# Kernel optimization log

Measured on AMD Instinct MI355X. Metric: run time of the kernel, lower is better.

Reference implementation:

```python
import jax, jax.numpy as jnp
import numpy as np

N_HEAD = 16
N_EMBD = 2048
B, S = 2, 2048


def setup_inputs() -> dict:
    key = jax.random.key(0)
    k1, k2, k3 = jax.random.split(key, 3)
    scale = 0.02
    return {
        "hidden_states": jax.random.normal(k1, (B, S, N_EMBD), dtype=jnp.float32),
        "attention_mask": jnp.ones((B, S), dtype=jnp.float32),
        "w_attn": jax.random.normal(k2, (N_EMBD, 3 * N_EMBD), dtype=jnp.float32) * scale,
        "b_attn": jnp.zeros((3 * N_EMBD,), dtype=jnp.float32),
        "w_proj": jax.random.normal(k3, (N_EMBD, N_EMBD), dtype=jnp.float32) * scale,
        "b_proj": jnp.zeros((N_EMBD,), dtype=jnp.float32),
    }


def reference(hidden_states, attention_mask, w_attn, b_attn, w_proj, b_proj):
    b, s, d = hidden_states.shape
    h = N_HEAD
    dh = d // h
    qkv = hidden_states @ w_attn + b_attn          # [b, s, 3d]
    q, k, v = jnp.split(qkv, 3, axis=-1)
    # [b, s, d] -> [b, h, s, dh]
    q = q.reshape(b, s, h, dh).transpose(0, 2, 1, 3)
    k = k.reshape(b, s, h, dh).transpose(0, 2, 1, 3)
    v = v.reshape(b, s, h, dh).transpose(0, 2, 1, 3)
    scores = jnp.einsum("bhqd,bhkd->bhqk", q, k) / jnp.sqrt(jnp.float32(dh))
    # padding mask: [b, s] -> additive bias [b, 1, 1, s]
    bias = (1.0 - attention_mask)[:, None, None, :] * -10000.0
    attn = jax.nn.softmax(scores + bias, axis=-1)   # dropout p=0 (eval)
    out = jnp.einsum("bhqk,bhkd->bhqd", attn, v)    # [b, h, s, dh]
    out = out.transpose(0, 2, 1, 3).reshape(b, s, d)
    return out @ w_proj + b_proj
```

## Files before the change

### kernel.cpp

```cpp
#include <hip/hip_runtime.h>
#include <stdint.h>

#define B_   2
#define S_   2048
#define D_   2048
#define NH_  16
#define DH_  128
#define N3_  6144

typedef unsigned short u16;
typedef __bf16 bf16x8 __attribute__((ext_vector_type(8)));
typedef float  f32x4  __attribute__((ext_vector_type(4)));

__device__ __forceinline__ u16 f2bf(float f) {
  union { float f; unsigned u; } v; v.f = f;
  unsigned u = v.u;
  return (u16)((u + 0x7FFFu + ((u >> 16) & 1u)) >> 16);
}

#define GL2LDS(gsrc, ldst)                                                              \
  __builtin_amdgcn_global_load_lds((const __attribute__((address_space(1))) void*)(gsrc), \
      (__attribute__((address_space(3))) void*)(ldst), 16, 0, 0)

__global__ void cvt_kernel(const float* __restrict__ in, u16* __restrict__ out, int n4) {
  int i = blockIdx.x * blockDim.x + threadIdx.x;
  int stride = gridDim.x * blockDim.x;
  for (; i < n4; i += stride) {
    float4 v = ((const float4*)in)[i];
    ushort4 o;
    o.x = f2bf(v.x); o.y = f2bf(v.y); o.z = f2bf(v.z); o.w = f2bf(v.w);
    ((ushort4*)out)[i] = o;
  }
}

__global__ void transpose_kernel(const float* __restrict__ in, u16* __restrict__ out,
                                 int K, int N) {
  __shared__ float tile[32][33];
  int tx = threadIdx.x, ty = threadIdx.y;
  int nx = blockIdx.x * 32, ky = blockIdx.y * 32;
#pragma unroll
  for (int j = 0; j < 32; j += 8)
    tile[ty + j][tx] = in[(size_t)(ky + ty + j) * N + nx + tx];
  __syncthreads();
#pragma unroll
  for (int j = 0; j < 32; j += 8)
    out[(size_t)(nx + ty + j) * K + ky + tx] = f2bf(tile[tx][ty + j]);
}

template <int KD>
__device__ __forceinline__ void gemm_core(const u16* __restrict__ A,
                                          const u16* __restrict__ BT,
                                          int m0, int n0, u16* As, u16* Bs,
                                          f32x4 acc[4][4]) {
  int t = threadIdx.x;
  int lane = t & 63, wv = t >> 6;
  int g = lane >> 4, lr = lane & 15;
  int wr = wv >> 1, wc = wv & 1;
  for (int k0 = 0; k0 < KD; k0 += 64) {
#pragma unroll
    for (int i = 0; i < 4; ++i) {
      int idx = i * 256 + t;
      int row = idx >> 3, slot = idx & 7;
      GL2LDS(A + (size_t)(m0 + row) * KD + k0 + ((slot ^ (row & 7)) * 8), As + idx * 8);
    }
#pragma unroll
    for (int i = 0; i < 4; ++i) {
      int idx = i * 256 + t;
      int row = idx >> 3, slot = idx & 7;
      GL2LDS(BT + (size_t)(n0 + row) * KD + k0 + ((slot ^ (row & 7)) * 8), Bs + idx * 8);
    }
    __syncthreads();
#pragma unroll
    for (int kk = 0; kk < 2; ++kk) {
      bf16x8 af[4], bfr[4];
#pragma unroll
      for (int m = 0; m < 4; ++m) {
        int r = wr * 64 + m * 16 + lr;
        af[m] = *reinterpret_cast<const bf16x8*>(As + r * 64 + ((((kk << 2) | g) ^ (r & 7)) * 8));
      }
#pragma unroll
      for (int n = 0; n < 4; ++n) {
        int r = wc * 64 + n * 16 + lr;
        bfr[n] = *reinterpret_cast<const bf16x8*>(Bs + r * 64 + ((((kk << 2) | g) ^ (r & 7)) * 8));
      }
#pragma unroll
      for (int m = 0; m < 4; ++m)
#pragma unroll
        for (int n = 0; n < 4; ++n)
          acc[m][n] = __builtin_amdgcn_mfma_f32_16x16x32_bf16(af[m], bfr[n], acc[m][n], 0, 0, 0);
    }
    __syncthreads();
  }
}

__global__ __launch_bounds__(256) void gemm_qkv_kernel(
    const u16* __restrict__ A, const u16* __restrict__ BT, const float* __restrict__ bias,
    u16* __restrict__ Qb, u16* __restrict__ Kb, u16* __restrict__ VTb) {
  __shared__ __attribute__((aligned(16))) u16 As[128 * 64];
  __shared__ __attribute__((aligned(16))) u16 Bs[128 * 64];
  f32x4 acc[4][4] = {};
  int m0 = blockIdx.y * 128, n0 = blockIdx.x * 128;
  gemm_core<2048>(A, BT, m0, n0, As, Bs, acc);
  int t = threadIdx.x, lane = t & 63, wv = t >> 6;
  int g = lane >> 4, lr = lane & 15, wr = wv >> 1, wc = wv & 1;
#pragma unroll
  for (int m = 0; m < 4; ++m) {
    int rowbase = m0 + wr * 64 + m * 16 + g * 4;
    int b = rowbase >> 11, s = rowbase & 2047;
#pragma unroll
    for (int n = 0; n < 4; ++n) {
      int col = n0 + wc * 64 + n * 16 + lr;
      float bv = bias[col];
      int sec = col >> 11;
      int within = col & 2047;
      int h = within >> 7, d = within & 127;
      if (sec < 2) {
        u16* dst = (sec == 0 ? Qb : Kb) + ((size_t)(b * NH_ + h) * S_ + s) * DH_ + d;
#pragma unroll
        for (int r = 0; r < 4; ++r) dst[(size_t)r * DH_] = f2bf(acc[m][n][r] + bv);
      } else {
        u16* dst = VTb + ((size_t)(b * NH_ + h) * DH_ + d) * S_ + s;
        ushort4 pk;
        pk.x = f2bf(acc[m][n][0] + bv); pk.y = f2bf(acc[m][n][1] + bv);
        pk.z = f2bf(acc[m][n][2] + bv); pk.w = f2bf(acc[m][n][3] + bv);
        *reinterpret_cast<ushort4*>(dst) = pk;
      }
    }
  }
}

__global__ __launch_bounds__(256) void gemm_proj_kernel(
    const u16* __restrict__ A, const u16* __restrict__ BT, const float* __restrict__ bias,
    float* __restrict__ out) {
  __shared__ __attribute__((aligned(16))) u16 As[128 * 64];
  __shared__ __attribute__((aligned(16))) u16 Bs[128 * 64];
  f32x4 acc[4][4] = {};
  int m0 = blockIdx.y * 128, n0 = blockIdx.x * 128;
  gemm_core<2048>(A, BT, m0, n0, As, Bs, acc);
  int t = threadIdx.x, lane = t & 63, wv = t >> 6;
  int g = lane >> 4, lr = lane & 15, wr = wv >> 1, wc = wv & 1;
#pragma unroll
  for (int m = 0; m < 4; ++m) {
    int rowbase = m0 + wr * 64 + m * 16 + g * 4;
#pragma unroll
    for (int n = 0; n < 4; ++n) {
      int col = n0 + wc * 64 + n * 16 + lr;
      float bv = bias[col];
      float* dst = out + (size_t)rowbase * D_ + col;
#pragma unroll
      for (int r = 0; r < 4; ++r) dst[(size_t)r * D_] = acc[m][n][r] + bv;
    }
  }
}

__global__ __launch_bounds__(256) void attn_kernel(
    const u16* __restrict__ Qb, const u16* __restrict__ Kb, const u16* __restrict__ VTb,
    const float* __restrict__ mask, u16* __restrict__ AO) {
  __shared__ __attribute__((aligned(16))) u16 Ks[64 * 128];
  __shared__ __attribute__((aligned(16))) u16 Vs[128 * 64];
  __shared__ __attribute__((aligned(16))) u16 Ps[4][16 * 64];
  int t = threadIdx.x, w = t >> 6, lane = t & 63;
  int g = lane >> 4, lr = lane & 15;
  int qt = blockIdx.x, bh = blockIdx.y;
  int b = bh >> 4, h = bh & 15;
  const u16* Qh = Qb + (size_t)bh * S_ * DH_;
  const u16* Kh = Kb + (size_t)bh * S_ * DH_;
  const u16* Vh = VTb + (size_t)bh * DH_ * S_;
  int q0 = qt * 64 + w * 16;

  bf16x8 aq[4];
#pragma unroll
  for (int kk = 0; kk < 4; ++kk)
    aq[kk] = *reinterpret_cast<const bf16x8*>(Qh + (size_t)(q0 + lr) * DH_ + kk * 32 + g * 8);

  f32x4 oacc[8] = {};
  float m_r[4], l_r[4];
#pragma unroll
  for (int r = 0; r < 4; ++r) { m_r[r] = -1e30f; l_r[r] = 0.f; }
  const float sc = 0.08838834764831845f;

  for (int s0 = 0; s0 < S_; s0 += 64) {
#pragma unroll
    for (int i = 0; i < 4; ++i) {
      int idx = i * 256 + t;
      int row = idx >> 4, slot = idx & 15;
      GL2LDS(Kh + (size_t)(s0 + row) * DH_ + ((slot ^ (row & 7)) * 8), Ks + idx * 8);
    }
#pragma unroll
    for (int i = 0; i < 4; ++i) {
      int idx = i * 256 + t;
      int row = idx >> 3, slot = idx & 7;
      GL2LDS(Vh + (size_t)row * S_ + s0 + ((slot ^ (row & 7)) * 8), Vs + idx * 8);
    }
    __syncthreads();

    f32x4 sacc[4] = {};
#pragma unroll
    for (int kk = 0; kk < 4; ++kk) {
#pragma unroll
      for (int n = 0; n < 4; ++n) {
        int c = lr + 16 * n;
        bf16x8 bk = *reinterpret_cast<const bf16x8*>(
            Ks + c * 128 + ((((kk << 2) | g) ^ (c & 7)) * 8));
        sacc[n] = __builtin_amdgcn_mfma_f32_16x16x32_bf16(aq[kk], bk, sacc[n], 0, 0, 0);
      }
    }

    float bias_n[4];
#pragma unroll
    for (int n = 0; n < 4; ++n)
      bias_n[n] = (1.0f - mask[b * S_ + s0 + lr + 16 * n]) * -10000.0f;

#pragma unroll
    for (int r = 0; r < 4; ++r) {
      float sv[4];
#pragma unroll
      for (int n = 0; n < 4; ++n) sv[n] = sacc[n][r] * sc + bias_n[n];
      float mx = fmaxf(fmaxf(sv[0], sv[1]), fmaxf(sv[2], sv[3]));
#pragma unroll
      for (int off = 1; off < 16; off <<= 1) mx = fmaxf(mx, __shfl_xor(mx, off));
      float mnew = fmaxf(m_r[r], mx);
      float f = __expf(m_r[r] - mnew);
      m_r[r] = mnew;
      float sum = 0.f;
      u16 pb[4];
#pragma unroll
      for (int n = 0; n < 4; ++n) { float p = __expf(sv[n] - mnew); sum += p; pb[n] = f2bf(p); }
#pragma unroll
      for (int off = 1; off < 16; off <<= 1) sum += __shfl_xor(sum, off);
      l_r[r] = l_r[r] * f + sum;
#pragma unroll
      for (int no = 0; no < 8; ++no) oacc[no][r] *= f;
      int prow = g * 4 + r;
#pragma unroll
      for (int n = 0; n < 4; ++n) {
        int col = lr + 16 * n;
        Ps[w][prow * 64 + ((((col >> 3) ^ (prow & 7)) << 3) + (col & 7))] = pb[n];
      }
    }

#pragma unroll
    for (int kk2 = 0; kk2 < 2; ++kk2) {
      bf16x8 ap = *reinterpret_cast<const bf16x8*>(
          &Ps[w][lr * 64 + ((((kk2 << 2) | g) ^ (lr & 7)) * 8)]);
#pragma unroll
      for (int no = 0; no < 8; ++no) {
        int d = lr + 16 * no;
        bf16x8 bv = *reinterpret_cast<const bf16x8*>(
            Vs + d * 64 + ((((kk2 << 2) | g) ^ (d & 7)) * 8));
        oacc[no] = __builtin_amdgcn_mfma_f32_16x16x32_bf16(ap, bv, oacc[no], 0, 0, 0);
      }
    }
    __syncthreads();
  }

#pragma unroll
  for (int r = 0; r < 4; ++r) {
    float inv = 1.0f / l_r[r];
    int qrow = q0 + g * 4 + r;
    u16* dst = AO + ((size_t)(b * S_ + qrow)) * D_ + h * DH_;
#pragma unroll
    for (int no = 0; no < 8; ++no) dst[lr + 16 * no] = f2bf(oacc[no][r] * inv);
  }
}

extern "C" void kernel_launch(void* const* d_in, const int* in_sizes, int n_in,
                              void* d_out, int out_size, void* d_ws, size_t ws_size,
                              hipStream_t stream) {
  const float* h_in   = (const float*)d_in[0];
  const float* mask   = (const float*)d_in[1];
  const float* w_attn = (const float*)d_in[2];
  const float* b_attn = (const float*)d_in[3];
  const float* w_proj = (const float*)d_in[4];
  const float* b_proj = (const float*)d_in[5];
  float* out = (float*)d_out;

  char* ws = (char*)d_ws;
  u16* Hb  = (u16*)(ws);
  u16* W1T = (u16*)(ws + 16777216);
  u16* W2T = (u16*)(ws + 41943040);
  u16* Qb  = (u16*)(ws + 50331648);
  u16* Kb  = (u16*)(ws + 67108864);
  u16* VTb = (u16*)(ws + 83886080);
  u16* AO  = Hb;

  cvt_kernel<<<2048, 256, 0, stream>>>(h_in, Hb, (B_ * S_ * D_) / 4);
  dim3 tb(32, 8);
  transpose_kernel<<<dim3(N3_ / 32, D_ / 32), tb, 0, stream>>>(w_attn, W1T, D_, N3_);
  transpose_kernel<<<dim3(D_ / 32, D_ / 32), tb, 0, stream>>>(w_proj, W2T, D_, D_);
  gemm_qkv_kernel<<<dim3(N3_ / 128, (B_ * S_) / 128), 256, 0, stream>>>(
      Hb, W1T, b_attn, Qb, Kb, VTb);
  attn_kernel<<<dim3(S_ / 64, B_ * NH_), 256, 0, stream>>>(Qb, Kb, VTb, mask, AO);
  gemm_proj_kernel<<<dim3(D_ / 128, (B_ * S_) / 128), 256, 0, stream>>>(AO, W2T, b_proj, out);
}
```

Before: 482.3 us.

## Double-buffer K/V in attention, fold scale into Q, lazy softmax rescale, swizzle blocks

```diff
diff --git a/kernel.cpp b/kernel.cpp
--- a/kernel.cpp
+++ b/kernel.cpp
@@ -12,15 +12,30 @@
 typedef __bf16 bf16x8 __attribute__((ext_vector_type(8)));
 typedef float  f32x4  __attribute__((ext_vector_type(4)));
 
+#define QSCALE   (0.08838834764831845f * 1.4426950408889634f)
+#define BIASF    (-10000.0f * 1.4426950408889634f)
+
 __device__ __forceinline__ u16 f2bf(float f) {
   union { float f; unsigned u; } v; v.f = f;
   unsigned u = v.u;
   return (u16)((u + 0x7FFFu + ((u >> 16) & 1u)) >> 16);
 }
 
+__device__ __forceinline__ float fast_exp2(float x) {
+  float r;
+  asm("v_exp_f32 %0, %1" : "=v"(r) : "v"(x));
+  return r;
+}
+
 #define GL2LDS(gsrc, ldst)                                                              \
   __builtin_amdgcn_global_load_lds((const __attribute__((address_space(1))) void*)(gsrc), \
       (__attribute__((address_space(3))) void*)(ldst), 16, 0, 0)
+
+__device__ __forceinline__ int swz_id() {
+  int id = blockIdx.y * gridDim.x + blockIdx.x;
+  int cpx = (gridDim.x * gridDim.y) >> 3;
+  return (id & 7) * cpx + (id >> 3);
+}
 
 __global__ void cvt_kernel(const float* __restrict__ in, u16* __restrict__ out, int n4) {
   int i = blockIdx.x * blockDim.x + threadIdx.x;
@@ -99,7 +114,8 @@
   __shared__ __attribute__((aligned(16))) u16 As[128 * 64];
   __shared__ __attribute__((aligned(16))) u16 Bs[128 * 64];
   f32x4 acc[4][4] = {};
-  int m0 = blockIdx.y * 128, n0 = blockIdx.x * 128;
+  int sw = swz_id();
+  int n0 = (sw % gridDim.x) * 128, m0 = (sw / gridDim.x) * 128;
   gemm_core<2048>(A, BT, m0, n0, As, Bs, acc);
   int t = threadIdx.x, lane = t & 63, wv = t >> 6;
   int g = lane >> 4, lr = lane & 15, wr = wv >> 1, wc = wv & 1;
@@ -115,9 +131,10 @@
       int within = col & 2047;
       int h = within >> 7, d = within & 127;
       if (sec < 2) {
+        float mult = (sec == 0) ? QSCALE : 1.0f;
         u16* dst = (sec == 0 ? Qb : Kb) + ((size_t)(b * NH_ + h) * S_ + s) * DH_ + d;
 #pragma unroll
-        for (int r = 0; r < 4; ++r) dst[(size_t)r * DH_] = f2bf(acc[m][n][r] + bv);
+        for (int r = 0; r < 4; ++r) dst[(size_t)r * DH_] = f2bf((acc[m][n][r] + bv) * mult);
       } else {
         u16* dst = VTb + ((size_t)(b * NH_ + h) * DH_ + d) * S_ + s;
         ushort4 pk;
@@ -135,7 +152,8 @@
   __shared__ __attribute__((aligned(16))) u16 As[128 * 64];
   __shared__ __attribute__((aligned(16))) u16 Bs[128 * 64];
   f32x4 acc[4][4] = {};
-  int m0 = blockIdx.y * 128, n0 = blockIdx.x * 128;
+  int sw = swz_id();
+  int n0 = (sw % gridDim.x) * 128, m0 = (sw / gridDim.x) * 128;
   gemm_core<2048>(A, BT, m0, n0, As, Bs, acc);
   int t = threadIdx.x, lane = t & 63, wv = t >> 6;
   int g = lane >> 4, lr = lane & 15, wr = wv >> 1, wc = wv & 1;
@@ -156,18 +174,24 @@
 __global__ __launch_bounds__(256) void attn_kernel(
     const u16* __restrict__ Qb, const u16* __restrict__ Kb, const u16* __restrict__ VTb,
     const float* __restrict__ mask, u16* __restrict__ AO) {
-  __shared__ __attribute__((aligned(16))) u16 Ks[64 * 128];
-  __shared__ __attribute__((aligned(16))) u16 Vs[128 * 64];
+  __shared__ __attribute__((aligned(16))) u16 Ks[2][64 * 128];
+  __shared__ __attribute__((aligned(16))) u16 Vs[2][128 * 64];
   __shared__ __attribute__((aligned(16))) u16 Ps[4][16 * 64];
+  __shared__ float bias_lds[S_];
+
   int t = threadIdx.x, w = t >> 6, lane = t & 63;
   int g = lane >> 4, lr = lane & 15;
-  int qt = blockIdx.x, bh = blockIdx.y;
-  int b = bh >> 4, h = bh & 15;
+  int sw = swz_id();
+  int qt = sw & 31, bh = sw >> 5;
+  int b = bh >> 4;
   const u16* Qh = Qb + (size_t)bh * S_ * DH_;
   const u16* Kh = Kb + (size_t)bh * S_ * DH_;
   const u16* Vh = VTb + (size_t)bh * DH_ * S_;
   int q0 = qt * 64 + w * 16;
 
+  for (int i = t; i < S_; i += 256)
+    bias_lds[i] = (1.0f - mask[b * S_ + i]) * BIASF;
+
   bf16x8 aq[4];
 #pragma unroll
   for (int kk = 0; kk < 4; ++kk)
@@ -177,22 +201,39 @@
   float m_r[4], l_r[4];
 #pragma unroll
   for (int r = 0; r < 4; ++r) { m_r[r] = -1e30f; l_r[r] = 0.f; }
-  const float sc = 0.08838834764831845f;
-
-  for (int s0 = 0; s0 < S_; s0 += 64) {
-#pragma unroll
-    for (int i = 0; i < 4; ++i) {
-      int idx = i * 256 + t;
-      int row = idx >> 4, slot = idx & 15;
-      GL2LDS(Kh + (size_t)(s0 + row) * DH_ + ((slot ^ (row & 7)) * 8), Ks + idx * 8);
-    }
-#pragma unroll
-    for (int i = 0; i < 4; ++i) {
-      int idx = i * 256 + t;
-      int row = idx >> 3, slot = idx & 7;
-      GL2LDS(Vh + (size_t)row * S_ + s0 + ((slot ^ (row & 7)) * 8), Vs + idx * 8);
-    }
-    __syncthreads();
+
+  __syncthreads();
+
+#define STAGE_KV(buf, s0base)                                                    \
+  {                                                                              \
+    _Pragma("unroll")                                                            \
+    for (int i = 0; i < 4; ++i) {                                                \
+      int idx = i * 256 + t;                                                     \
+      int row = idx >> 4, slot = idx & 15;                                       \
+      GL2LDS(Kh + (size_t)((s0base) + row) * DH_ + ((slot ^ (row & 7)) * 8),     \
+             &Ks[buf][idx * 8]);                                                 \
+    }                                                                            \
+    _Pragma("unroll")                                                            \
+    for (int i = 0; i < 4; ++i) {                                                \
+      int idx = i * 256 + t;                                                     \
+      int row = idx >> 3, slot = idx & 7;                                        \
+      GL2LDS(Vh + (size_t)row * S_ + (s0base) + ((slot ^ (row & 7)) * 8),        \
+             &Vs[buf][idx * 8]);                                                 \
+    }                                                                            \
+  }
+
+  STAGE_KV(0, 0);
+  const int NT = S_ / 64;
+  for (int it = 0; it < NT; ++it) {
+    int cur = it & 1;
+    if (it + 1 < NT) {
+      STAGE_KV(cur ^ 1, (it + 1) * 64);
+      asm volatile("s_waitcnt vmcnt(8)" ::: "memory");
+    } else {
+      asm volatile("s_waitcnt vmcnt(0)" ::: "memory");
+    }
+    __builtin_amdgcn_s_barrier();
+    __builtin_amdgcn_sched_barrier(0);
 
     f32x4 sacc[4] = {};
 #pragma unroll
@@ -201,41 +242,44 @@
       for (int n = 0; n < 4; ++n) {
         int c = lr + 16 * n;
         bf16x8 bk = *reinterpret_cast<const bf16x8*>(
-            Ks + c * 128 + ((((kk << 2) | g) ^ (c & 7)) * 8));
+            &Ks[cur][c * 128 + ((((kk << 2) | g) ^ (c & 7)) * 8)]);
         sacc[n] = __builtin_amdgcn_mfma_f32_16x16x32_bf16(aq[kk], bk, sacc[n], 0, 0, 0);
       }
     }
 
-    float bias_n[4];
-#pragma unroll
-    for (int n = 0; n < 4; ++n)
-      bias_n[n] = (1.0f - mask[b * S_ + s0 + lr + 16 * n]) * -10000.0f;
-
+    int s0 = it * 64;
+    float sv[4][4], mx[4];
 #pragma unroll
     for (int r = 0; r < 4; ++r) {
-      float sv[4];
-#pragma unroll
-      for (int n = 0; n < 4; ++n) sv[n] = sacc[n][r] * sc + bias_n[n];
-      float mx = fmaxf(fmaxf(sv[0], sv[1]), fmaxf(sv[2], sv[3]));
-#pragma unroll
-      for (int off = 1; off < 16; off <<= 1) mx = fmaxf(mx, __shfl_xor(mx, off));
-      float mnew = fmaxf(m_r[r], mx);
-      float f = __expf(m_r[r] - mnew);
-      m_r[r] = mnew;
-      float sum = 0.f;
-      u16 pb[4];
-#pragma unroll
-      for (int n = 0; n < 4; ++n) { float p = __expf(sv[n] - mnew); sum += p; pb[n] = f2bf(p); }
-#pragma unroll
-      for (int off = 1; off < 16; off <<= 1) sum += __shfl_xor(sum, off);
-      l_r[r] = l_r[r] * f + sum;
-#pragma unroll
-      for (int no = 0; no < 8; ++no) oacc[no][r] *= f;
+#pragma unroll
+      for (int n = 0; n < 4; ++n) sv[r][n] = sacc[n][r] + bias_lds[s0 + lr + 16 * n];
+      float m2 = fmaxf(fmaxf(sv[r][0], sv[r][1]), fmaxf(sv[r][2], sv[r][3]));
+#pragma unroll
+      for (int off = 1; off < 16; off <<= 1) m2 = fmaxf(m2, __shfl_xor(m2, off));
+      mx[r] = m2;
+    }
+    float gmax = fmaxf(fmaxf(mx[0] - m_r[0], mx[1] - m_r[1]),
+                       fmaxf(mx[2] - m_r[2], mx[3] - m_r[3]));
+    if (__any(gmax > 8.f)) {
+#pragma unroll
+      for (int r = 0; r < 4; ++r) {
+        float mnew = fmaxf(m_r[r], mx[r]);
+        float f = fast_exp2(m_r[r] - mnew);
+        m_r[r] = mnew;
+        l_r[r] *= f;
+#pragma unroll
+        for (int no = 0; no < 8; ++no) oacc[no][r] *= f;
+      }
+    }
+#pragma unroll
+    for (int r = 0; r < 4; ++r) {
       int prow = g * 4 + r;
 #pragma unroll
       for (int n = 0; n < 4; ++n) {
+        float p = fast_exp2(sv[r][n] - m_r[r]);
+        l_r[r] += p;
         int col = lr + 16 * n;
-        Ps[w][prow * 64 + ((((col >> 3) ^ (prow & 7)) << 3) + (col & 7))] = pb[n];
+        Ps[w][prow * 64 + ((((col >> 3) ^ (prow & 7)) << 3) + (col & 7))] = f2bf(p);
       }
     }
 
@@ -247,17 +291,23 @@
       for (int no = 0; no < 8; ++no) {
         int d = lr + 16 * no;
         bf16x8 bv = *reinterpret_cast<const bf16x8*>(
-            Vs + d * 64 + ((((kk2 << 2) | g) ^ (d & 7)) * 8));
+            &Vs[cur][d * 64 + ((((kk2 << 2) | g) ^ (d & 7)) * 8)]);
         oacc[no] = __builtin_amdgcn_mfma_f32_16x16x32_bf16(ap, bv, oacc[no], 0, 0, 0);
       }
     }
-    __syncthreads();
-  }
+    __builtin_amdgcn_sched_barrier(0);
+    __builtin_amdgcn_s_barrier();
+  }
+#undef STAGE_KV
 
 #pragma unroll
   for (int r = 0; r < 4; ++r) {
-    float inv = 1.0f / l_r[r];
+    float s = l_r[r];
+#pragma unroll
+    for (int off = 1; off < 16; off <<= 1) s += __shfl_xor(s, off);
+    float inv = 1.0f / s;
     int qrow = q0 + g * 4 + r;
+    int h = bh & 15;
     u16* dst = AO + ((size_t)(b * S_ + qrow)) * D_ + h * DH_;
 #pragma unroll
     for (int no = 0; no < 8; ++no) dst[lr + 16 * no] = f2bf(oacc[no][r] * inv);
```

After: 468.2 us. -2.9%, faster.
